# Kernel tuning notes

Measured on AMD Instinct MI355X. Metric: run time of the kernel, lower is better.

Reference implementation:

```python
import jax, jax.numpy as jnp
import numpy as np

L = 2          # num_layers
D = 2048       # embed_dim
HQ = 16        # num_q_heads
HK = 4         # num_kv_heads
HD = D // HQ   # head_size = 128
G = HQ // HK   # q_to_kv_ratio = 4
P = 8192       # embed_dim_proj
V = 32000      # vocab_size
B = 1
S = 2048
EPS = 1e-5
THETA = 500000.0
NEG = -1e30


def setup_inputs() -> dict:
    key = jax.random.key(0)
    ks = jax.random.split(key, 8)
    s = 0.02
    return {
        "tokens": jax.random.randint(ks[0], (B, S), 0, V, dtype=jnp.int32),
        "embed": jax.random.normal(ks[1], (V, D), jnp.float32) * s,
        "attn_norm_w": jnp.ones((L, D), jnp.float32),
        "qkv_w": jax.random.normal(ks[2], (L, D, D + 2 * HK * HD), jnp.float32) * s,
        "attn_out_w": jax.random.normal(ks[3], (L, D, D), jnp.float32) * s,
        "mlp_norm_w": jnp.ones((L, D), jnp.float32),
        "mlp_in_w": jax.random.normal(ks[4], (L, D, 2 * P), jnp.float32) * s,
        "mlp_out_w": jax.random.normal(ks[5], (L, P, D), jnp.float32) * s,
        "final_norm_w": jnp.ones((D,), jnp.float32),
        "lm_head_w": jax.random.normal(ks[6], (D, V), jnp.float32) * s,
    }


def _rms(x, w):
    return w * (x * jax.lax.rsqrt(jnp.mean(x * x, axis=-1, keepdims=True) + EPS))


def _rope_cos_sin():
    inv = 1.0 / (THETA ** (jnp.arange(0, HD, 2, dtype=jnp.float32) / HD))  # [HD/2]
    ang = jnp.arange(S, dtype=jnp.float32)[:, None] * inv[None, :]         # [S, HD/2]
    return jnp.cos(ang), jnp.sin(ang)


def _rope(t, cos, sin):
    # t: [B,S,H,HD]; interleaved complex rotation on (even, odd) pairs
    x = t.reshape(t.shape[:-1] + (HD // 2, 2))
    x0, x1 = x[..., 0], x[..., 1]
    c = cos[None, :, None, :]
    sn = sin[None, :, None, :]
    out = jnp.stack([x0 * c - x1 * sn, x0 * sn + x1 * c], axis=-1)
    return out.reshape(t.shape)


def _layer(x, nw1, wqkv, wo, nw2, wi, wmo, cos, sin, mask):
    # attention block (pre-norm, residual)
    h = _rms(x, nw1)
    qkv = h @ wqkv
    q = qkv[..., :D].reshape(B, S, HQ, HD)
    k = qkv[..., D:D + HK * HD].reshape(B, S, HK, HD)
    v = qkv[..., D + HK * HD:].reshape(B, S, HK, HD)
    q = _rope(q, cos, sin)
    k = _rope(k, cos, sin)
    # GQA: repeat_interleave along head dim
    k = jnp.repeat(k, G, axis=2)
    v = jnp.repeat(v, G, axis=2)
    scores = jnp.einsum('bqhd,bkhd->bhqk', q, k) / np.float32(np.sqrt(HD))
    scores = jnp.where(mask, scores, NEG)
    attn = jax.nn.softmax(scores, axis=-1)
    o = jnp.einsum('bhqk,bkhd->bqhd', attn, v).reshape(B, S, D)
    x = x + o @ wo
    # SwiGLU block (pre-norm, residual)
    h = _rms(x, nw2)
    gu = h @ wi
    gate, up = gu[..., :P], gu[..., P:]
    x = x + (jax.nn.silu(gate) * up) @ wmo
    return x


def reference(tokens, embed, attn_norm_w, qkv_w, attn_out_w, mlp_norm_w,
              mlp_in_w, mlp_out_w, final_norm_w, lm_head_w):
    cos, sin = _rope_cos_sin()
    mask = jnp.tril(jnp.ones((S, S), dtype=bool))  # offset=0 prefill -> causal
    x = embed[tokens]  # [B,S,D]
    for i in range(L):
        x = _layer(x, attn_norm_w[i], qkv_w[i], attn_out_w[i],
                   mlp_norm_w[i], mlp_in_w[i], mlp_out_w[i], cos, sin, mask)
    return _rms(x, final_norm_w) @ lm_head_w  # [B,S,V]
```

## Files before the change

### kernel.cpp

```cpp
#include <hip/hip_runtime.h>
#include <math.h>

#define S_LEN 2048
#define DMODEL 2048
#define NHQ 16
#define NHK 4
#define HDIM 128
#define PDIM 8192
#define VOCAB 32000
#define NQKV 3072
#define EPSI 1e-5f

typedef unsigned short u16;
typedef unsigned int u32;
typedef __bf16 bf16x8 __attribute__((ext_vector_type(8)));
typedef float f32x4 __attribute__((ext_vector_type(4)));

__device__ __forceinline__ u16 f2bf(float f){
  u32 u = __builtin_bit_cast(u32, f);
  u += 0x7fffu + ((u >> 16) & 1u);
  return (u16)(u >> 16);
}
__device__ __forceinline__ float bf2f(u16 h){
  u32 u = ((u32)h) << 16;
  return __builtin_bit_cast(float, u);
}
__device__ __forceinline__ bf16x8 ld8(const u16* p){
  return __builtin_bit_cast(bf16x8, *(const uint4*)p);
}
__device__ __forceinline__ f32x4 mfma16(bf16x8 a, bf16x8 b, f32x4 c){
  return __builtin_amdgcn_mfma_f32_16x16x32_bf16(a, b, c, 0, 0, 0);
}

#define GLOAD_LDS16(gp, lp) __builtin_amdgcn_global_load_lds( \
    (__attribute__((address_space(1))) void*)(gp), \
    (__attribute__((address_space(3))) void*)(lp), 16, 0, 0)

__device__ __forceinline__ bf16x8 lds_frag(const u16* Lb, int R, int g){
  const int Rp = R >> 1;
  const int s8 = (((R & 1) << 2) | g) ^ (Rp & 7);
  return ld8(Lb + Rp * 64 + s8 * 8);
}
__device__ __forceinline__ void stage_sw(const u16* base, long row0, int K, int kt,
                                         int q, u16* Ldst_waveuniform){
  const int Rp = q >> 3;
  const int u = (q & 7) ^ (Rp & 7);
  const int R = (Rp << 1) | (u >> 2);
  const u16* gp = base + (row0 + R) * (long)K + kt + ((u & 3) << 3);
  GLOAD_LDS16(gp, Ldst_waveuniform);
}

__global__ void k_embed(const int* __restrict__ tok, const float* __restrict__ emb,
                        float* __restrict__ x){
  const int s = blockIdx.x, t = threadIdx.x;
  const long r = tok[s];
  const float4* src = (const float4*)(emb + r * DMODEL);
  float4* dst = (float4*)(x + (long)s * DMODEL);
  dst[t] = src[t];
  dst[t + 256] = src[t + 256];
}

__global__ void k_rmsnorm(const float* __restrict__ x, const float* __restrict__ w,
                          u16* __restrict__ out){
  const int s = blockIdx.x, t = threadIdx.x;
  const float4* xr = (const float4*)(x + (long)s * DMODEL);
  const float4 a = xr[t], b = xr[t + 256];
  float ss = a.x*a.x + a.y*a.y + a.z*a.z + a.w*a.w
           + b.x*b.x + b.y*b.y + b.z*b.z + b.w*b.w;
  #pragma unroll
  for (int off = 32; off > 0; off >>= 1) ss += __shfl_down(ss, off, 64);
  __shared__ float part[4];
  if ((t & 63) == 0) part[t >> 6] = ss;
  __syncthreads();
  const float r = rsqrtf((part[0] + part[1] + part[2] + part[3]) * (1.f / 2048.f) + EPSI);
  const float4* wr = (const float4*)w;
  const float4 wa = wr[t], wb = wr[t + 256];
  uint2 ua, ub;
  ua.x = (u32)f2bf(a.x*r*wa.x) | ((u32)f2bf(a.y*r*wa.y) << 16);
  ua.y = (u32)f2bf(a.z*r*wa.z) | ((u32)f2bf(a.w*r*wa.w) << 16);
  ub.x = (u32)f2bf(b.x*r*wb.x) | ((u32)f2bf(b.y*r*wb.y) << 16);
  ub.y = (u32)f2bf(b.z*r*wb.z) | ((u32)f2bf(b.w*r*wb.w) << 16);
  *(uint2*)(out + (long)s * DMODEL + 4 * t) = ua;
  *(uint2*)(out + (long)s * DMODEL + 1024 + 4 * t) = ub;
}

__global__ __launch_bounds__(256) void k_convT(const float* __restrict__ W,
                                               u16* __restrict__ Wt, int N, int K){
  const int n0 = blockIdx.x * 64, k0 = blockIdx.y * 64;
  const int t = threadIdx.x;
  __shared__ u16 T[64][72];
  const int r = t >> 4, c = (t & 15) << 2;
  #pragma unroll
  for (int p = 0; p < 4; ++p){
    const int k = p * 16 + r;
    const float4 v = *(const float4*)(W + (long)(k0 + k) * N + n0 + c);
    T[c + 0][k] = f2bf(v.x);
    T[c + 1][k] = f2bf(v.y);
    T[c + 2][k] = f2bf(v.z);
    T[c + 3][k] = f2bf(v.w);
  }
  __syncthreads();
  const int nr = t >> 3, kc = (t & 7) << 3;
  #pragma unroll
  for (int p = 0; p < 2; ++p){
    const int n = p * 32 + nr;
    *(uint4*)(Wt + (long)(n0 + n) * K + k0 + kc) = *(const uint4*)(&T[n][kc]);
  }
}

__global__ __launch_bounds__(256) void k_transV(const u16* __restrict__ qkv,
                                                u16* __restrict__ vT){
  const int s0 = blockIdx.x * 64, d0 = blockIdx.y * 64, kh = blockIdx.z;
  const int t = threadIdx.x;
  __shared__ u16 T[64][72];
  #pragma unroll
  for (int p = 0; p < 4; ++p){
    const int s = p * 16 + (t >> 4);
    const int c = (t & 15) * 4;
    const uint2 v = *(const uint2*)(qkv + (long)(s0 + s) * NQKV + DMODEL + 512 + kh * HDIM + d0 + c);
    T[c + 0][s] = (u16)(v.x);
    T[c + 1][s] = (u16)(v.x >> 16);
    T[c + 2][s] = (u16)(v.y);
    T[c + 3][s] = (u16)(v.y >> 16);
  }
  __syncthreads();
  #pragma unroll
  for (int p = 0; p < 2; ++p){
    const int d = p * 32 + (t >> 3);
    *(uint4*)(vT + ((long)kh * HDIM + d0 + d) * S_LEN + s0 + (t & 7) * 8) =
        *(const uint4*)(&T[d][(t & 7) * 8]);
  }
}

template<int OUT_BF16, int RES>
__global__ __launch_bounds__(256) void k_gemm(const u16* __restrict__ A, const u16* __restrict__ Bt,
                                              void* C, const float* Rs,
                                              int M, int N, int K){
  const int bm = blockIdx.x, bn = blockIdx.y;
  const int t = threadIdx.x;
  const int w = t >> 6, lane = t & 63, l15 = lane & 15, g = lane >> 4;
  const int wr = w >> 1, wc = w & 1;
  __shared__ u16 As[4096];
  __shared__ u16 Bs[4096];
  f32x4 acc[4][4] = {};
  const long arow = (long)bm * 128;
  const long brow = (long)bn * 128;
  for (int kt = 0; kt < K; kt += 32){
    __syncthreads();
    #pragma unroll
    for (int c = 0; c < 2; ++c){
      const int q0 = ((w << 1) | c) << 6;
      const int q  = q0 | lane;
      stage_sw(A,  arow, K, kt, q, As + q0 * 8);
      stage_sw(Bt, brow, K, kt, q, Bs + q0 * 8);
    }
    __syncthreads();
    bf16x8 af[4], bfr[4];
    #pragma unroll
    for (int i = 0; i < 4; ++i)
      af[i] = lds_frag(As, wr * 64 + i * 16 + l15, g);
    #pragma unroll
    for (int i = 0; i < 4; ++i)
      bfr[i] = lds_frag(Bs, wc * 64 + i * 16 + l15, g);
    #pragma unroll
    for (int mi = 0; mi < 4; ++mi)
      #pragma unroll
      for (int ni = 0; ni < 4; ++ni)
        acc[mi][ni] = mfma16(af[mi], bfr[ni], acc[mi][ni]);
  }
  const int row0 = bm * 128 + wr * 64, col0 = bn * 128 + wc * 64;
  #pragma unroll
  for (int mi = 0; mi < 4; ++mi){
    #pragma unroll
    for (int ni = 0; ni < 4; ++ni){
      #pragma unroll
      for (int r = 0; r < 4; ++r){
        const long ri = row0 + mi * 16 + g * 4 + r;
        const long ci = col0 + ni * 16 + l15;
        float v = acc[mi][ni][r];
        if (RES) v += Rs[ri * N + ci];
        if (OUT_BF16) ((u16*)C)[ri * N + ci] = f2bf(v);
        else          ((float*)C)[ri * N + ci] = v;
      }
    }
  }
}

template<int OUT_BF16>
__global__ __launch_bounds__(512, 2) void k_gemm256(const u16* __restrict__ A,
                                                    const u16* __restrict__ Bt,
                                                    void* C, int M, int N, int K){
  __shared__ u16 L[65536];
  const int t = threadIdx.x;
  const int w = t >> 6, lane = t & 63, l15 = lane & 15, g = lane >> 4;
  const int wr = w >> 2, wc = w & 3;
  const int nbm = M >> 8;
  int id = blockIdx.x;
  {
    const int cpx = gridDim.x >> 3;
    id = (id & 7) * cpx + (id >> 3);
  }
  const int bm = id % nbm, bn = id / nbm;
  const int NT = K >> 5;

  const int Rp0 = t >> 3;
  const int u0  = (t & 7) ^ (Rp0 & 7);
  const int R0  = (Rp0 << 1) | (u0 >> 2);
  const u16* pA0 = A  + ((long)bm * 256 + R0) * (long)K + ((u0 & 3) << 3);
  const u16* pB0 = Bt + ((long)bn * 256 + R0) * (long)K + ((u0 & 3) << 3);
  const u16* pA1 = pA0 + (long)128 * K;
  const u16* pB1 = pB0 + (long)128 * K;
  const int w0 = (t & ~63) * 8;

  auto stageA = [&](int slot){
    u16* ldsA = L + slot * 8192;
    GLOAD_LDS16(pA0, ldsA + w0);
    GLOAD_LDS16(pA1, ldsA + 4096 + w0);
    pA0 += 32; pA1 += 32;
  };
  auto stageB = [&](int slot){
    u16* ldsB = L + 32768 + slot * 8192;
    GLOAD_LDS16(pB0, ldsB + w0);
    GLOAD_LDS16(pB1, ldsB + 4096 + w0);
    pB0 += 32; pB1 += 32;
  };

  #pragma unroll
  for (int i = 0; i < 3; ++i){ stageA(i); stageB(i); }
  asm volatile("s_waitcnt vmcnt(8)" ::: "memory");
  __builtin_amdgcn_s_barrier();

  f32x4 acc[8][4] = {};
  for (int tt = 0; tt < NT; ++tt){
    const u16* sA = L + (tt & 3) * 8192;
    const u16* sB = L + 32768 + (tt & 3) * 8192;
    bf16x8 af0[4], bfr[4];
    #pragma unroll
    for (int j = 0; j < 4; ++j)
      af0[j] = lds_frag(sA, wr * 128 + j * 16 + l15, g);
    #pragma unroll
    for (int n = 0; n < 4; ++n)
      bfr[n] = lds_frag(sB, wc * 64 + n * 16 + l15, g);
    if (tt + 3 < NT) stageA((tt + 3) & 3);
    asm volatile("s_waitcnt lgkmcnt(0)" ::: "memory");
    __builtin_amdgcn_s_barrier();
    __builtin_amdgcn_s_setprio(1);
    #pragma unroll
    for (int mi = 0; mi < 4; ++mi)
      #pragma unroll
      for (int ni = 0; ni < 4; ++ni)
        acc[mi][ni] = mfma16(af0[mi], bfr[ni], acc[mi][ni]);
    __builtin_amdgcn_s_setprio(0);
    bf16x8 af1[4];
    #pragma unroll
    for (int j = 0; j < 4; ++j)
      af1[j] = lds_frag(sA, wr * 128 + 64 + j * 16 + l15, g);
    if (tt + 3 < NT) stageB((tt + 3) & 3);
    asm volatile("s_waitcnt lgkmcnt(0)" ::: "memory");
    if (tt + 1 < NT){
      if (tt + 3 < NT)      asm volatile("s_waitcnt vmcnt(8)" ::: "memory");
      else if (tt + 2 < NT) asm volatile("s_waitcnt vmcnt(4)" ::: "memory");
      else                  asm volatile("s_waitcnt vmcnt(0)" ::: "memory");
    }
    __builtin_amdgcn_s_barrier();
    __builtin_amdgcn_s_setprio(1);
    #pragma unroll
    for (int mi = 0; mi < 4; ++mi)
      #pragma unroll
      for (int ni = 0; ni < 4; ++ni)
        acc[4 + mi][ni] = mfma16(af1[mi], bfr[ni], acc[4 + mi][ni]);
    __builtin_amdgcn_s_setprio(0);
  }
  const int row0 = bm * 256 + wr * 128, col0 = bn * 256 + wc * 64;
  #pragma unroll
  for (int mi = 0; mi < 8; ++mi){
    #pragma unroll
    for (int ni = 0; ni < 4; ++ni){
      #pragma unroll
      for (int r = 0; r < 4; ++r){
        const long ri = row0 + mi * 16 + g * 4 + r;
        const long ci = col0 + ni * 16 + l15;
        const float v = acc[mi][ni][r];
        if (OUT_BF16) ((u16*)C)[ri * N + ci] = f2bf(v);
        else          ((float*)C)[ri * N + ci] = v;
      }
    }
  }
}

__global__ void k_rope(u16* __restrict__ qkv){
  const int idx = blockIdx.x * 256 + threadIdx.x;
  const int i = idx & 63;
  const int head = (idx >> 6) % 20;
  const int s = idx / (64 * 20);
  const long base = (long)s * NQKV + (head < NHQ ? head * HDIM : DMODEL + (head - NHQ) * HDIM);
  u32* p = (u32*)(qkv + base + 2 * i);
  const u32 v = *p;
  const float x0 = bf2f((u16)(v & 0xffffu)), x1 = bf2f((u16)(v >> 16));
  const float ang = (float)s * exp2f(-0.29580575889569023f * (float)i);
  float sn, cs;
  sincosf(ang, &sn, &cs);
  const float y0 = x0 * cs - x1 * sn;
  const float y1 = x0 * sn + x1 * cs;
  *p = (u32)f2bf(y0) | ((u32)f2bf(y1) << 16);
}

__global__ __launch_bounds__(256) void k_attn(const u16* __restrict__ qkv,
                                              const u16* __restrict__ vT,
                                              u16* __restrict__ o){
  const int qb = blockIdx.x, h = blockIdx.y;
  const int kh = h >> 2;
  const int t = threadIdx.x, w = t >> 6, lane = t & 63, l15 = lane & 15, g = lane >> 4;
  __shared__ u16 Ks[2][8192];
  __shared__ u16 Vs[2][8192];
  __shared__ u16 Ps[4][16 * 72];
  const int q0 = qb * 64 + w * 16;
  bf16x8 aq[4];
  #pragma unroll
  for (int d0 = 0; d0 < 4; ++d0)
    aq[d0] = ld8(qkv + (long)(q0 + l15) * NQKV + h * HDIM + d0 * 32 + g * 8);
  f32x4 acc_o[8] = {};
  float mst[4], lst[4];
  #pragma unroll
  for (int r = 0; r < 4; ++r){ mst[r] = -1e30f; lst[r] = 0.f; }
  const float scale = 0.08838834764831843f;

  auto stageK = [&](int kt, int b){
    #pragma unroll
    for (int p = 0; p < 4; ++p){
      const int q = p * 256 + t;
      const int r = q >> 4, u = q & 15;
      const u16* gp = qkv + (long)(kt * 64 + r) * NQKV + DMODEL + kh * HDIM + ((u ^ (r & 15)) << 3);
      GLOAD_LDS16(gp, Ks[b] + (p * 256 + (t & ~63)) * 8);
    }
  };
  auto stageV = [&](int kt, int b){
    #pragma unroll
    for (int p = 0; p < 4; ++p){
      const int q = p * 256 + t;
      const int r = q >> 3, u = q & 7;
      const u16* gp = vT + ((long)kh * HDIM + r) * S_LEN + kt * 64 + ((u ^ (r & 7)) << 3);
      GLOAD_LDS16(gp, Vs[b] + (p * 256 + (t & ~63)) * 8);
    }
  };

  const int nkt = qb + 1;
  stageK(0, 0); stageV(0, 0);
  for (int kt = 0; kt < nkt; ++kt){
    const int kv0 = kt << 6;
    __builtin_amdgcn_s_barrier();
    if (kt + 1 < nkt){
      stageK(kt + 1, (kt + 1) & 1);
      stageV(kt + 1, (kt + 1) & 1);
      asm volatile("s_waitcnt vmcnt(8)" ::: "memory");
    } else {
      asm volatile("s_waitcnt vmcnt(0)" ::: "memory");
    }
    __builtin_amdgcn_s_barrier();
    const u16* K_ = Ks[kt & 1];
    const u16* V_ = Vs[kt & 1];
    f32x4 sacc[4] = {};
    #pragma unroll
    for (int d0 = 0; d0 < 4; ++d0){
      #pragma unroll
      for (int j = 0; j < 4; ++j){
        const bf16x8 bk = ld8(K_ + (j * 16 + l15) * 128 + ((((d0 << 2) | g) ^ l15) << 3));
        sacc[j] = mfma16(aq[d0], bk, sacc[j]);
      }
    }
    float p[4][4], scl[4];
    #pragma unroll
    for (int r = 0; r < 4; ++r){
      const int qrow = q0 + g * 4 + r;
      float mx = -1e30f;
      #pragma unroll
      for (int j = 0; j < 4; ++j){
        float sv = sacc[j][r] * scale;
        sv = (kv0 + j * 16 + l15 <= qrow) ? sv : -1e30f;
        p[j][r] = sv;
        mx = fmaxf(mx, sv);
      }
      #pragma unroll
      for (int off = 1; off < 16; off <<= 1) mx = fmaxf(mx, __shfl_xor(mx, off, 64));
      const float mnew = fmaxf(mst[r], mx);
      scl[r] = __expf(mst[r] - mnew);
      float rs = 0.f;
      #pragma unroll
      for (int j = 0; j < 4; ++j){ p[j][r] = __expf(p[j][r] - mnew); rs += p[j][r]; }
      #pragma unroll
      for (int off = 1; off < 16; off <<= 1) rs += __shfl_xor(rs, off, 64);
      lst[r] = lst[r] * scl[r] + rs;
      mst[r] = mnew;
    }
    #pragma unroll
    for (int n = 0; n < 8; ++n)
      #pragma unroll
      for (int r = 0; r < 4; ++r)
        acc_o[n][r] *= scl[r];
    #pragma unroll
    for (int j = 0; j < 4; ++j)
      #pragma unroll
      for (int r = 0; r < 4; ++r)
        Ps[w][(g * 4 + r) * 72 + j * 16 + l15] = f2bf(p[j][r]);
    #pragma unroll
    for (int kk = 0; kk < 2; ++kk){
      const bf16x8 pa = ld8(Ps[w] + l15 * 72 + kk * 32 + g * 8);
      #pragma unroll
      for (int n = 0; n < 8; ++n){
        const int row = n * 16 + l15;
        const bf16x8 bv = ld8(V_ + row * 64 + ((((kk << 2) | g) ^ (l15 & 7)) << 3));
        acc_o[n] = mfma16(pa, bv, acc_o[n]);
      }
    }
    asm volatile("s_waitcnt lgkmcnt(0)" ::: "memory");
  }
  #pragma unroll
  for (int n = 0; n < 8; ++n){
    #pragma unroll
    for (int r = 0; r < 4; ++r){
      const float ov = acc_o[n][r] / lst[r];
      o[(long)(q0 + g * 4 + r) * DMODEL + h * HDIM + n * 16 + l15] = f2bf(ov);
    }
  }
}

__global__ void k_swiglu(const u16* __restrict__ gu, u16* __restrict__ out){
  const long idx = ((long)blockIdx.x * 256 + threadIdx.x) * 8;
  const long s = idx >> 13;
  const int j = (int)(idx & 8191);
  const u16* gp = gu + s * 16384 + j;
  const uint4 gv = *(const uint4*)gp;
  const uint4 uv = *(const uint4*)(gp + PDIM);
  const u32 gw[4] = {gv.x, gv.y, gv.z, gv.w};
  const u32 uw[4] = {uv.x, uv.y, uv.z, uv.w};
  u32 ow[4];
  #pragma unroll
  for (int k = 0; k < 4; ++k){
    const float g0 = bf2f((u16)(gw[k] & 0xffffu)), g1 = bf2f((u16)(gw[k] >> 16));
    const float u0 = bf2f((u16)(uw[k] & 0xffffu)), u1 = bf2f((u16)(uw[k] >> 16));
    const float s0 = g0 / (1.f + __expf(-g0)) * u0;
    const float s1 = g1 / (1.f + __expf(-g1)) * u1;
    ow[k] = (u32)f2bf(s0) | ((u32)f2bf(s1) << 16);
  }
  uint4 ro; ro.x = ow[0]; ro.y = ow[1]; ro.z = ow[2]; ro.w = ow[3];
  *(uint4*)(out + idx) = ro;
}

extern "C" void kernel_launch(void* const* d_in, const int* in_sizes, int n_in,
                              void* d_out, int out_size, void* d_ws, size_t ws_size,
                              hipStream_t stream){
  const int*   tokens       = (const int*)d_in[0];
  const float* embed        = (const float*)d_in[1];
  const float* attn_norm_w  = (const float*)d_in[2];
  const float* qkv_w        = (const float*)d_in[3];
  const float* attn_out_w   = (const float*)d_in[4];
  const float* mlp_norm_w   = (const float*)d_in[5];
  const float* mlp_in_w     = (const float*)d_in[6];
  const float* mlp_out_w    = (const float*)d_in[7];
  const float* final_norm_w = (const float*)d_in[8];
  const float* lm_head_w    = (const float*)d_in[9];

  char* ws = (char*)d_ws;
  float* xf  = (float*)(ws);
  u16* hbf   = (u16*)(ws + 16777216);
  u16* qkvb  = (u16*)(ws + 25165824);
  u16* obf   = (u16*)(ws + 37748736);
  u16* gub   = (u16*)(ws + 46137344);
  u16* hb2   = (u16*)(ws + 113246208);
  u16* wbuf  = (u16*)(ws + 146800640);
  u16* vTb   = (u16*)(ws + 277872640);

  k_embed<<<S_LEN, 256, 0, stream>>>(tokens, embed, xf);
  for (int l = 0; l < 2; ++l){
    k_rmsnorm<<<S_LEN, 256, 0, stream>>>(xf, attn_norm_w + (long)l * DMODEL, hbf);
    k_convT<<<dim3(NQKV/64, DMODEL/64), 256, 0, stream>>>(
        qkv_w + (long)l * DMODEL * NQKV, wbuf, NQKV, DMODEL);
    k_gemm<1,0><<<dim3(S_LEN/128, NQKV/128), 256, 0, stream>>>(
        hbf, wbuf, qkvb, nullptr, S_LEN, NQKV, DMODEL);
    k_rope<<<(S_LEN * 20 * 64) / 256, 256, 0, stream>>>(qkvb);
    k_transV<<<dim3(S_LEN/64, 2, 4), 256, 0, stream>>>(qkvb, vTb);
    k_attn<<<dim3(S_LEN/64, NHQ), 256, 0, stream>>>(qkvb, vTb, obf);
    k_convT<<<dim3(DMODEL/64, DMODEL/64), 256, 0, stream>>>(
        attn_out_w + (long)l * DMODEL * DMODEL, wbuf, DMODEL, DMODEL);
    k_gemm<0,1><<<dim3(S_LEN/128, DMODEL/128), 256, 0, stream>>>(
        obf, wbuf, xf, xf, S_LEN, DMODEL, DMODEL);
    k_rmsnorm<<<S_LEN, 256, 0, stream>>>(xf, mlp_norm_w + (long)l * DMODEL, hbf);
    k_convT<<<dim3((2*PDIM)/64, DMODEL/64), 256, 0, stream>>>(
        mlp_in_w + (long)l * DMODEL * 2 * PDIM, wbuf, 2*PDIM, DMODEL);
    k_gemm256<1><<<(S_LEN/256) * ((2*PDIM)/256), 512, 0, stream>>>(
        hbf, wbuf, gub, S_LEN, 2*PDIM, DMODEL);
    k_swiglu<<<(S_LEN * PDIM / 8) / 256, 256, 0, stream>>>(gub, hb2);
    k_convT<<<dim3(DMODEL/64, PDIM/64), 256, 0, stream>>>(
        mlp_out_w + (long)l * PDIM * DMODEL, wbuf, DMODEL, PDIM);
    k_gemm<0,1><<<dim3(S_LEN/128, DMODEL/128), 256, 0, stream>>>(
        hb2, wbuf, xf, xf, S_LEN, DMODEL, PDIM);
  }
  k_rmsnorm<<<S_LEN, 256, 0, stream>>>(xf, final_norm_w, hbf);
  k_convT<<<dim3(VOCAB/64, DMODEL/64), 256, 0, stream>>>(lm_head_w, wbuf, VOCAB, DMODEL);
  k_gemm256<0><<<(S_LEN/256) * (VOCAB/256), 512, 0, stream>>>(
      hbf, wbuf, (float*)d_out, S_LEN, VOCAB, DMODEL);
}
```

Measured before the change: 1.535 ms.

## Restructure 256-tile GEMM pipeline to K=64 double-buffer and add grouped block mapping

The 256x256 GEMM mainloop moves from a 4-slot, K=32 ring buffer to a double-buffered K=64 scheme. Each iteration runs four MFMA phases separated by explicit barriers, and global-to-LDS loads for the next stage are interleaved with the fragment reads. Both GEMM kernels now use a shared XCD-aware grouped tile mapping (map_bmn) so blocks on the same XCD share A-row panels and get better L2 reuse. The small GEMM launches change from a 2D to a 1D grid with group sizes passed in. The added barriers and reduced prefetch depth could expose memory latency, and the mapping assumes the grid size is divisible by 8.

```diff
diff --git a/kernel.cpp b/kernel.cpp
--- a/kernel.cpp
+++ b/kernel.cpp
@@ -48,6 +48,16 @@
   const int R = (Rp << 1) | (u >> 2);
   const u16* gp = base + (row0 + R) * (long)K + kt + ((u & 3) << 3);
   GLOAD_LDS16(gp, Ldst_waveuniform);
+}
+
+__device__ __forceinline__ void map_bmn(int id0, int nwg, int nbn, int G,
+                                        int& bm, int& bn){
+  const int cpx = nwg >> 3;
+  const int id = (id0 & 7) * cpx + (id0 >> 3);
+  const int bmi = id % G;
+  const int r2 = id / G;
+  bn = r2 % nbn;
+  bm = (r2 / nbn) * G + bmi;
 }
 
 __global__ void k_embed(const int* __restrict__ tok, const float* __restrict__ emb,
@@ -135,8 +145,9 @@
 template<int OUT_BF16, int RES>
 __global__ __launch_bounds__(256) void k_gemm(const u16* __restrict__ A, const u16* __restrict__ Bt,
                                               void* C, const float* Rs,
-                                              int M, int N, int K){
-  const int bm = blockIdx.x, bn = blockIdx.y;
+                                              int M, int N, int K, int nbn, int G){
+  int bm, bn;
+  map_bmn(blockIdx.x, gridDim.x, nbn, G, bm, bn);
   const int t = threadIdx.x;
   const int w = t >> 6, lane = t & 63, l15 = lane & 15, g = lane >> 4;
   const int wr = w >> 1, wc = w & 1;
@@ -194,14 +205,10 @@
   const int t = threadIdx.x;
   const int w = t >> 6, lane = t & 63, l15 = lane & 15, g = lane >> 4;
   const int wr = w >> 2, wc = w & 3;
-  const int nbm = M >> 8;
-  int id = blockIdx.x;
-  {
-    const int cpx = gridDim.x >> 3;
-    id = (id & 7) * cpx + (id >> 3);
-  }
-  const int bm = id % nbm, bn = id / nbm;
-  const int NT = K >> 5;
+  const int nbn = N >> 8;
+  int bm, bn;
+  map_bmn(blockIdx.x, gridDim.x, nbn, 2, bm, bn);
+  const int NT = K >> 6;
 
   const int Rp0 = t >> 3;
   const int u0  = (t & 7) ^ (Rp0 & 7);
@@ -212,64 +219,95 @@
   const u16* pB1 = pB0 + (long)128 * K;
   const int w0 = (t & ~63) * 8;
 
-  auto stageA = [&](int slot){
-    u16* ldsA = L + slot * 8192;
-    GLOAD_LDS16(pA0, ldsA + w0);
-    GLOAD_LDS16(pA1, ldsA + 4096 + w0);
-    pA0 += 32; pA1 += 32;
-  };
-  auto stageB = [&](int slot){
-    u16* ldsB = L + 32768 + slot * 8192;
-    GLOAD_LDS16(pB0, ldsB + w0);
-    GLOAD_LDS16(pB1, ldsB + 4096 + w0);
-    pB0 += 32; pB1 += 32;
-  };
-
-  #pragma unroll
-  for (int i = 0; i < 3; ++i){ stageA(i); stageB(i); }
-  asm volatile("s_waitcnt vmcnt(8)" ::: "memory");
+  GLOAD_LDS16(pA0,      L + w0);
+  GLOAD_LDS16(pA1,      L + w0 + 4096);
+  GLOAD_LDS16(pB0,      L + 32768 + w0);
+  GLOAD_LDS16(pB1,      L + 32768 + w0 + 4096);
+  GLOAD_LDS16(pA0 + 32, L + 8192 + w0);
+  GLOAD_LDS16(pA1 + 32, L + 8192 + w0 + 4096);
+  GLOAD_LDS16(pB0 + 32, L + 32768 + 8192 + w0);
+  GLOAD_LDS16(pB1 + 32, L + 32768 + 8192 + w0 + 4096);
+  pA0 += 64; pA1 += 64; pB0 += 64; pB1 += 64;
+  asm volatile("s_waitcnt vmcnt(4)" ::: "memory");
   __builtin_amdgcn_s_barrier();
 
   f32x4 acc[8][4] = {};
   for (int tt = 0; tt < NT; ++tt){
-    const u16* sA = L + (tt & 3) * 8192;
-    const u16* sB = L + 32768 + (tt & 3) * 8192;
-    bf16x8 af0[4], bfr[4];
-    #pragma unroll
-    for (int j = 0; j < 4; ++j)
-      af0[j] = lds_frag(sA, wr * 128 + j * 16 + l15, g);
-    #pragma unroll
-    for (int n = 0; n < 4; ++n)
-      bfr[n] = lds_frag(sB, wc * 64 + n * 16 + l15, g);
-    if (tt + 3 < NT) stageA((tt + 3) & 3);
+    const int c = tt & 1, d = c ^ 1;
+    const u16* LA0 = L + c * 16384;
+    const u16* LA1 = LA0 + 8192;
+    const u16* LB0 = L + 32768 + c * 16384;
+    const u16* LB1 = LB0 + 8192;
+    u16* SA0 = L + d * 16384;
+    u16* SA1 = SA0 + 8192;
+    u16* SB0 = L + 32768 + d * 16384;
+    u16* SB1 = SB0 + 8192;
+    const bool more = (tt + 1 < NT);
+    bf16x8 afr[4], bfr[4];
+    #pragma unroll
+    for (int i = 0; i < 4; ++i) afr[i] = lds_frag(LA0, wr * 128 + i * 16 + l15, g);
+    #pragma unroll
+    for (int i = 0; i < 4; ++i) bfr[i] = lds_frag(LB0, wc * 64 + i * 16 + l15, g);
+    if (more){ GLOAD_LDS16(pA0, SA0 + w0); GLOAD_LDS16(pA1, SA0 + w0 + 4096); }
+    __builtin_amdgcn_s_barrier();
     asm volatile("s_waitcnt lgkmcnt(0)" ::: "memory");
-    __builtin_amdgcn_s_barrier();
+    __builtin_amdgcn_sched_barrier(0);
     __builtin_amdgcn_s_setprio(1);
     #pragma unroll
     for (int mi = 0; mi < 4; ++mi)
       #pragma unroll
       for (int ni = 0; ni < 4; ++ni)
-        acc[mi][ni] = mfma16(af0[mi], bfr[ni], acc[mi][ni]);
+        acc[mi][ni] = mfma16(afr[mi], bfr[ni], acc[mi][ni]);
     __builtin_amdgcn_s_setprio(0);
-    bf16x8 af1[4];
-    #pragma unroll
-    for (int j = 0; j < 4; ++j)
-      af1[j] = lds_frag(sA, wr * 128 + 64 + j * 16 + l15, g);
-    if (tt + 3 < NT) stageB((tt + 3) & 3);
+    __builtin_amdgcn_s_barrier();
+    #pragma unroll
+    for (int i = 0; i < 4; ++i) afr[i] = lds_frag(LA0, wr * 128 + 64 + i * 16 + l15, g);
+    if (more){ GLOAD_LDS16(pB0, SB0 + w0); GLOAD_LDS16(pB1, SB0 + w0 + 4096); }
+    if (more) asm volatile("s_waitcnt vmcnt(4)" ::: "memory");
+    else      asm volatile("s_waitcnt vmcnt(0)" ::: "memory");
+    __builtin_amdgcn_s_barrier();
     asm volatile("s_waitcnt lgkmcnt(0)" ::: "memory");
-    if (tt + 1 < NT){
-      if (tt + 3 < NT)      asm volatile("s_waitcnt vmcnt(8)" ::: "memory");
-      else if (tt + 2 < NT) asm volatile("s_waitcnt vmcnt(4)" ::: "memory");
-      else                  asm volatile("s_waitcnt vmcnt(0)" ::: "memory");
-    }
-    __builtin_amdgcn_s_barrier();
+    __builtin_amdgcn_sched_barrier(0);
     __builtin_amdgcn_s_setprio(1);
     #pragma unroll
     for (int mi = 0; mi < 4; ++mi)
       #pragma unroll
       for (int ni = 0; ni < 4; ++ni)
-        acc[4 + mi][ni] = mfma16(af1[mi], bfr[ni], acc[4 + mi][ni]);
+        acc[4 + mi][ni] = mfma16(afr[mi], bfr[ni], acc[4 + mi][ni]);
     __builtin_amdgcn_s_setprio(0);
+    __builtin_amdgcn_s_barrier();
+    #pragma unroll
+    for (int i = 0; i < 4; ++i) afr[i] = lds_frag(LA1, wr * 128 + i * 16 + l15, g);
+    #pragma unroll
+    for (int i = 0; i < 4; ++i) bfr[i] = lds_frag(LB1, wc * 64 + i * 16 + l15, g);
+    if (more){ GLOAD_LDS16(pA0 + 32, SA1 + w0); GLOAD_LDS16(pA1 + 32, SA1 + w0 + 4096); }
+    __builtin_amdgcn_s_barrier();
+    asm volatile("s_waitcnt lgkmcnt(0)" ::: "memory");
+    __builtin_amdgcn_sched_barrier(0);
+    __builtin_amdgcn_s_setprio(1);
+    #pragma unroll
+    for (int mi = 0; mi < 4; ++mi)
+      #pragma unroll
+      for (int ni = 0; ni < 4; ++ni)
+        acc[mi][ni] = mfma16(afr[mi], bfr[ni], acc[mi][ni]);
+    __builtin_amdgcn_s_setprio(0);
+    __builtin_amdgcn_s_barrier();
+    #pragma unroll
+    for (int i = 0; i < 4; ++i) afr[i] = lds_frag(LA1, wr * 128 + 64 + i * 16 + l15, g);
+    if (more){ GLOAD_LDS16(pB0 + 32, SB1 + w0); GLOAD_LDS16(pB1 + 32, SB1 + w0 + 4096); }
+    if (more) asm volatile("s_waitcnt vmcnt(4)" ::: "memory");
+    __builtin_amdgcn_s_barrier();
+    asm volatile("s_waitcnt lgkmcnt(0)" ::: "memory");
+    __builtin_amdgcn_sched_barrier(0);
+    __builtin_amdgcn_s_setprio(1);
+    #pragma unroll
+    for (int mi = 0; mi < 4; ++mi)
+      #pragma unroll
+      for (int ni = 0; ni < 4; ++ni)
+        acc[4 + mi][ni] = mfma16(afr[mi], bfr[ni], acc[4 + mi][ni]);
+    __builtin_amdgcn_s_setprio(0);
+    __builtin_amdgcn_s_barrier();
+    pA0 += 64; pA1 += 64; pB0 += 64; pB1 += 64;
   }
   const int row0 = bm * 256 + wr * 128, col0 = bn * 256 + wc * 64;
   #pragma unroll
@@ -475,15 +513,15 @@
     k_rmsnorm<<<S_LEN, 256, 0, stream>>>(xf, attn_norm_w + (long)l * DMODEL, hbf);
     k_convT<<<dim3(NQKV/64, DMODEL/64), 256, 0, stream>>>(
         qkv_w + (long)l * DMODEL * NQKV, wbuf, NQKV, DMODEL);
-    k_gemm<1,0><<<dim3(S_LEN/128, NQKV/128), 256, 0, stream>>>(
-        hbf, wbuf, qkvb, nullptr, S_LEN, NQKV, DMODEL);
+    k_gemm<1,0><<<(S_LEN/128) * (NQKV/128), 256, 0, stream>>>(
+        hbf, wbuf, qkvb, nullptr, S_LEN, NQKV, DMODEL, NQKV/128, 4);
     k_rope<<<(S_LEN * 20 * 64) / 256, 256, 0, stream>>>(qkvb);
     k_transV<<<dim3(S_LEN/64, 2, 4), 256, 0, stream>>>(qkvb, vTb);
     k_attn<<<dim3(S_LEN/64, NHQ), 256, 0, stream>>>(qkvb, vTb, obf);
     k_convT<<<dim3(DMODEL/64, DMODEL/64), 256, 0, stream>>>(
         attn_out_w + (long)l * DMODEL * DMODEL, wbuf, DMODEL, DMODEL);
-    k_gemm<0,1><<<dim3(S_LEN/128, DMODEL/128), 256, 0, stream>>>(
-        obf, wbuf, xf, xf, S_LEN, DMODEL, DMODEL);
+    k_gemm<0,1><<<(S_LEN/128) * (DMODEL/128), 256, 0, stream>>>(
+        obf, wbuf, xf, xf, S_LEN, DMODEL, DMODEL, DMODEL/128, 4);
     k_rmsnorm<<<S_LEN, 256, 0, stream>>>(xf, mlp_norm_w + (long)l * DMODEL, hbf);
     k_convT<<<dim3((2*PDIM)/64, DMODEL/64), 256, 0, stream>>>(
         mlp_in_w + (long)l * DMODEL * 2 * PDIM, wbuf, 2*PDIM, DMODEL);
@@ -492,8 +530,8 @@
     k_swiglu<<<(S_LEN * PDIM / 8) / 256, 256, 0, stream>>>(gub, hb2);
     k_convT<<<dim3(DMODEL/64, PDIM/64), 256, 0, stream>>>(
         mlp_out_w + (long)l * PDIM * DMODEL, wbuf, DMODEL, PDIM);
-    k_gemm<0,1><<<dim3(S_LEN/128, DMODEL/128), 256, 0, stream>>>(
-        hb2, wbuf, xf, xf, S_LEN, DMODEL, PDIM);
+    k_gemm<0,1><<<(S_LEN/128) * (DMODEL/128), 256, 0, stream>>>(
+        hb2, wbuf, xf, xf, S_LEN, DMODEL, PDIM, DMODEL/128, 2);
   }
   k_rmsnorm<<<S_LEN, 256, 0, stream>>>(xf, final_norm_w, hbf);
   k_convT<<<dim3(VOCAB/64, DMODEL/64), 256, 0, stream>>>(lm_head_w, wbuf, VOCAB, DMODEL);
```

After: 1.543 ms. No clear change (+0.5%).

## Add XCD-aware block remapping, persistent 256 GEMM, and heavy-first attention ordering

Applied to the files above, without the earlier changes.

Remaps GEMM block indices so that blocks landing on the same XCD (chiplet) share A/B tiles through grouped M-tiles, which is meant to improve L2 reuse. Turns the 256x256 GEMM into a persistent kernel: 256 workgroups each hold one M-tile fixed and loop over N-tiles with stride 32. Attention blocks are reassigned so that each XCD handles heads sharing a KV head, and query blocks are scheduled longest-first (causal) to reduce tail imbalance. In exchange, the persistent loop adds a per-tile prologue with no overlap between tiles and fixes the grid at 256, which may underfill the GPU or load-imbalance on the vocab GEMM (125 N-tiles over 32 slots).

```diff
diff --git a/kernel.cpp b/kernel.cpp
--- a/kernel.cpp
+++ b/kernel.cpp
@@ -48,6 +48,16 @@
   const int R = (Rp << 1) | (u >> 2);
   const u16* gp = base + (row0 + R) * (long)K + kt + ((u & 3) << 3);
   GLOAD_LDS16(gp, Ldst_waveuniform);
+}
+
+__device__ __forceinline__ void map_bmn(int id0, int nwg, int nbn, int G,
+                                        int& bm, int& bn){
+  const int cpx = nwg >> 3;
+  const int id = (id0 & 7) * cpx + (id0 >> 3);
+  const int bmi = id % G;
+  const int r2 = id / G;
+  bn = r2 % nbn;
+  bm = (r2 / nbn) * G + bmi;
 }
 
 __global__ void k_embed(const int* __restrict__ tok, const float* __restrict__ emb,
@@ -135,8 +145,9 @@
 template<int OUT_BF16, int RES>
 __global__ __launch_bounds__(256) void k_gemm(const u16* __restrict__ A, const u16* __restrict__ Bt,
                                               void* C, const float* Rs,
-                                              int M, int N, int K){
-  const int bm = blockIdx.x, bn = blockIdx.y;
+                                              int M, int N, int K, int nbn, int G){
+  int bm, bn;
+  map_bmn(blockIdx.x, gridDim.x, nbn, G, bm, bn);
   const int t = threadIdx.x;
   const int w = t >> 6, lane = t & 63, l15 = lane & 15, g = lane >> 4;
   const int wr = w >> 1, wc = w & 1;
@@ -187,102 +198,102 @@
 }
 
 template<int OUT_BF16>
-__global__ __launch_bounds__(512, 2) void k_gemm256(const u16* __restrict__ A,
-                                                    const u16* __restrict__ Bt,
-                                                    void* C, int M, int N, int K){
+__global__ __launch_bounds__(512, 2) void k_gemm256p(const u16* __restrict__ A,
+                                                     const u16* __restrict__ Bt,
+                                                     void* C, int M, int N, int K,
+                                                     int nbn){
   __shared__ u16 L[65536];
   const int t = threadIdx.x;
   const int w = t >> 6, lane = t & 63, l15 = lane & 15, g = lane >> 4;
   const int wr = w >> 2, wc = w & 3;
-  const int nbm = M >> 8;
-  int id = blockIdx.x;
-  {
-    const int cpx = gridDim.x >> 3;
-    id = (id & 7) * cpx + (id >> 3);
-  }
-  const int bm = id % nbm, bn = id / nbm;
+  const int bm   = blockIdx.x & 7;
+  const int slot = blockIdx.x >> 3;
   const int NT = K >> 5;
 
   const int Rp0 = t >> 3;
   const int u0  = (t & 7) ^ (Rp0 & 7);
   const int R0  = (Rp0 << 1) | (u0 >> 2);
-  const u16* pA0 = A  + ((long)bm * 256 + R0) * (long)K + ((u0 & 3) << 3);
-  const u16* pB0 = Bt + ((long)bn * 256 + R0) * (long)K + ((u0 & 3) << 3);
-  const u16* pA1 = pA0 + (long)128 * K;
-  const u16* pB1 = pB0 + (long)128 * K;
+  const int kcol0 = (u0 & 3) << 3;
+  const u16* pA0base = A + ((long)bm * 256 + R0) * (long)K + kcol0;
+  const u16* pA1base = pA0base + (long)128 * K;
   const int w0 = (t & ~63) * 8;
 
-  auto stageA = [&](int slot){
-    u16* ldsA = L + slot * 8192;
-    GLOAD_LDS16(pA0, ldsA + w0);
-    GLOAD_LDS16(pA1, ldsA + 4096 + w0);
-    pA0 += 32; pA1 += 32;
-  };
-  auto stageB = [&](int slot){
-    u16* ldsB = L + 32768 + slot * 8192;
-    GLOAD_LDS16(pB0, ldsB + w0);
-    GLOAD_LDS16(pB1, ldsB + 4096 + w0);
-    pB0 += 32; pB1 += 32;
-  };
-
-  #pragma unroll
-  for (int i = 0; i < 3; ++i){ stageA(i); stageB(i); }
-  asm volatile("s_waitcnt vmcnt(8)" ::: "memory");
-  __builtin_amdgcn_s_barrier();
-
-  f32x4 acc[8][4] = {};
-  for (int tt = 0; tt < NT; ++tt){
-    const u16* sA = L + (tt & 3) * 8192;
-    const u16* sB = L + 32768 + (tt & 3) * 8192;
-    bf16x8 af0[4], bfr[4];
-    #pragma unroll
-    for (int j = 0; j < 4; ++j)
-      af0[j] = lds_frag(sA, wr * 128 + j * 16 + l15, g);
-    #pragma unroll
-    for (int n = 0; n < 4; ++n)
-      bfr[n] = lds_frag(sB, wc * 64 + n * 16 + l15, g);
-    if (tt + 3 < NT) stageA((tt + 3) & 3);
-    asm volatile("s_waitcnt lgkmcnt(0)" ::: "memory");
+  for (int bn = slot; bn < nbn; bn += 32){
+    const u16* pA0 = pA0base;
+    const u16* pA1 = pA1base;
+    const u16* pB0 = Bt + ((long)bn * 256 + R0) * (long)K + kcol0;
+    const u16* pB1 = pB0 + (long)128 * K;
+
+    auto stageA = [&](int s){
+      u16* d = L + s * 8192;
+      GLOAD_LDS16(pA0, d + w0); GLOAD_LDS16(pA1, d + 4096 + w0);
+      pA0 += 32; pA1 += 32;
+    };
+    auto stageB = [&](int s){
+      u16* d = L + 32768 + s * 8192;
+      GLOAD_LDS16(pB0, d + w0); GLOAD_LDS16(pB1, d + 4096 + w0);
+      pB0 += 32; pB1 += 32;
+    };
+
     __builtin_amdgcn_s_barrier();
-    __builtin_amdgcn_s_setprio(1);
-    #pragma unroll
-    for (int mi = 0; mi < 4; ++mi)
-      #pragma unroll
-      for (int ni = 0; ni < 4; ++ni)
-        acc[mi][ni] = mfma16(af0[mi], bfr[ni], acc[mi][ni]);
-    __builtin_amdgcn_s_setprio(0);
-    bf16x8 af1[4];
-    #pragma unroll
-    for (int j = 0; j < 4; ++j)
-      af1[j] = lds_frag(sA, wr * 128 + 64 + j * 16 + l15, g);
-    if (tt + 3 < NT) stageB((tt + 3) & 3);
-    asm volatile("s_waitcnt lgkmcnt(0)" ::: "memory");
-    if (tt + 1 < NT){
-      if (tt + 3 < NT)      asm volatile("s_waitcnt vmcnt(8)" ::: "memory");
-      else if (tt + 2 < NT) asm volatile("s_waitcnt vmcnt(4)" ::: "memory");
-      else                  asm volatile("s_waitcnt vmcnt(0)" ::: "memory");
-    }
+    stageA(0); stageB(0); stageA(1); stageB(1); stageA(2); stageB(2);
+    asm volatile("s_waitcnt vmcnt(8)" ::: "memory");
     __builtin_amdgcn_s_barrier();
-    __builtin_amdgcn_s_setprio(1);
-    #pragma unroll
-    for (int mi = 0; mi < 4; ++mi)
-      #pragma unroll
-      for (int ni = 0; ni < 4; ++ni)
-        acc[4 + mi][ni] = mfma16(af1[mi], bfr[ni], acc[4 + mi][ni]);
-    __builtin_amdgcn_s_setprio(0);
-  }
-  const int row0 = bm * 256 + wr * 128, col0 = bn * 256 + wc * 64;
-  #pragma unroll
-  for (int mi = 0; mi < 8; ++mi){
-    #pragma unroll
-    for (int ni = 0; ni < 4; ++ni){
-      #pragma unroll
-      for (int r = 0; r < 4; ++r){
-        const long ri = row0 + mi * 16 + g * 4 + r;
-        const long ci = col0 + ni * 16 + l15;
-        const float v = acc[mi][ni][r];
-        if (OUT_BF16) ((u16*)C)[ri * N + ci] = f2bf(v);
-        else          ((float*)C)[ri * N + ci] = v;
+
+    f32x4 acc[8][4] = {};
+    for (int tt = 0; tt < NT; ++tt){
+      const u16* sA = L + (tt & 3) * 8192;
+      const u16* sB = L + 32768 + (tt & 3) * 8192;
+      bf16x8 af0[4], bfr[4];
+      #pragma unroll
+      for (int j = 0; j < 4; ++j)
+        af0[j] = lds_frag(sA, wr * 128 + j * 16 + l15, g);
+      #pragma unroll
+      for (int n = 0; n < 4; ++n)
+        bfr[n] = lds_frag(sB, wc * 64 + n * 16 + l15, g);
+      if (tt + 3 < NT) stageA((tt + 3) & 3);
+      asm volatile("s_waitcnt lgkmcnt(0)" ::: "memory");
+      __builtin_amdgcn_s_barrier();
+      __builtin_amdgcn_s_setprio(1);
+      #pragma unroll
+      for (int mi = 0; mi < 4; ++mi)
+        #pragma unroll
+        for (int ni = 0; ni < 4; ++ni)
+          acc[mi][ni] = mfma16(af0[mi], bfr[ni], acc[mi][ni]);
+      __builtin_amdgcn_s_setprio(0);
+      bf16x8 af1[4];
+      #pragma unroll
+      for (int j = 0; j < 4; ++j)
+        af1[j] = lds_frag(sA, wr * 128 + 64 + j * 16 + l15, g);
+      if (tt + 3 < NT) stageB((tt + 3) & 3);
+      asm volatile("s_waitcnt lgkmcnt(0)" ::: "memory");
+      if (tt + 1 < NT){
+        if (tt + 3 < NT)      asm volatile("s_waitcnt vmcnt(8)" ::: "memory");
+        else if (tt + 2 < NT) asm volatile("s_waitcnt vmcnt(4)" ::: "memory");
+        else                  asm volatile("s_waitcnt vmcnt(0)" ::: "memory");
+      }
+      __builtin_amdgcn_s_barrier();
+      __builtin_amdgcn_s_setprio(1);
+      #pragma unroll
+      for (int mi = 0; mi < 4; ++mi)
+        #pragma unroll
+        for (int ni = 0; ni < 4; ++ni)
+          acc[4 + mi][ni] = mfma16(af1[mi], bfr[ni], acc[4 + mi][ni]);
+      __builtin_amdgcn_s_setprio(0);
+    }
+    const int row0 = bm * 256 + wr * 128, col0 = bn * 256 + wc * 64;
+    #pragma unroll
+    for (int mi = 0; mi < 8; ++mi){
+      #pragma unroll
+      for (int ni = 0; ni < 4; ++ni){
+        #pragma unroll
+        for (int r = 0; r < 4; ++r){
+          const long ri = row0 + mi * 16 + g * 4 + r;
+          const long ci = col0 + ni * 16 + l15;
+          const float v = acc[mi][ni][r];
+          if (OUT_BF16) ((u16*)C)[ri * N + ci] = f2bf(v);
+          else          ((float*)C)[ri * N + ci] = v;
+        }
       }
     }
   }
@@ -308,8 +319,11 @@
 __global__ __launch_bounds__(256) void k_attn(const u16* __restrict__ qkv,
                                               const u16* __restrict__ vT,
                                               u16* __restrict__ o){
-  const int qb = blockIdx.x, h = blockIdx.y;
-  const int kh = h >> 2;
+  const int id = blockIdx.x;
+  const int xcd = id & 7, j = id >> 3;
+  const int kh = xcd >> 1;
+  const int h  = (kh << 2) + ((xcd & 1) << 1) + (j & 1);
+  const int qb = 31 - (j >> 1);
   const int t = threadIdx.x, w = t >> 6, lane = t & 63, l15 = lane & 15, g = lane >> 4;
   __shared__ u16 Ks[2][8192];
   __shared__ u16 Vs[2][8192];
@@ -363,9 +377,9 @@
     #pragma unroll
     for (int d0 = 0; d0 < 4; ++d0){
       #pragma unroll
-      for (int j = 0; j < 4; ++j){
-        const bf16x8 bk = ld8(K_ + (j * 16 + l15) * 128 + ((((d0 << 2) | g) ^ l15) << 3));
-        sacc[j] = mfma16(aq[d0], bk, sacc[j]);
+      for (int j2 = 0; j2 < 4; ++j2){
+        const bf16x8 bk = ld8(K_ + (j2 * 16 + l15) * 128 + ((((d0 << 2) | g) ^ l15) << 3));
+        sacc[j2] = mfma16(aq[d0], bk, sacc[j2]);
       }
     }
     float p[4][4], scl[4];
@@ -374,10 +388,10 @@
       const int qrow = q0 + g * 4 + r;
       float mx = -1e30f;
       #pragma unroll
-      for (int j = 0; j < 4; ++j){
-        float sv = sacc[j][r] * scale;
-        sv = (kv0 + j * 16 + l15 <= qrow) ? sv : -1e30f;
-        p[j][r] = sv;
+      for (int j2 = 0; j2 < 4; ++j2){
+        float sv = sacc[j2][r] * scale;
+        sv = (kv0 + j2 * 16 + l15 <= qrow) ? sv : -1e30f;
+        p[j2][r] = sv;
         mx = fmaxf(mx, sv);
       }
       #pragma unroll
@@ -386,7 +400,7 @@
       scl[r] = __expf(mst[r] - mnew);
       float rs = 0.f;
       #pragma unroll
-      for (int j = 0; j < 4; ++j){ p[j][r] = __expf(p[j][r] - mnew); rs += p[j][r]; }
+      for (int j2 = 0; j2 < 4; ++j2){ p[j2][r] = __expf(p[j2][r] - mnew); rs += p[j2][r]; }
       #pragma unroll
       for (int off = 1; off < 16; off <<= 1) rs += __shfl_xor(rs, off, 64);
       lst[r] = lst[r] * scl[r] + rs;
@@ -398,10 +412,10 @@
       for (int r = 0; r < 4; ++r)
         acc_o[n][r] *= scl[r];
     #pragma unroll
-    for (int j = 0; j < 4; ++j)
+    for (int j2 = 0; j2 < 4; ++j2)
       #pragma unroll
       for (int r = 0; r < 4; ++r)
-        Ps[w][(g * 4 + r) * 72 + j * 16 + l15] = f2bf(p[j][r]);
+        Ps[w][(g * 4 + r) * 72 + j2 * 16 + l15] = f2bf(p[j2][r]);
     #pragma unroll
     for (int kk = 0; kk < 2; ++kk){
       const bf16x8 pa = ld8(Ps[w] + l15 * 72 + kk * 32 + g * 8);
@@ -475,28 +489,28 @@
     k_rmsnorm<<<S_LEN, 256, 0, stream>>>(xf, attn_norm_w + (long)l * DMODEL, hbf);
     k_convT<<<dim3(NQKV/64, DMODEL/64), 256, 0, stream>>>(
         qkv_w + (long)l * DMODEL * NQKV, wbuf, NQKV, DMODEL);
-    k_gemm<1,0><<<dim3(S_LEN/128, NQKV/128), 256, 0, stream>>>(
-        hbf, wbuf, qkvb, nullptr, S_LEN, NQKV, DMODEL);
+    k_gemm<1,0><<<(S_LEN/128) * (NQKV/128), 256, 0, stream>>>(
+        hbf, wbuf, qkvb, nullptr, S_LEN, NQKV, DMODEL, NQKV/128, 4);
     k_rope<<<(S_LEN * 20 * 64) / 256, 256, 0, stream>>>(qkvb);
     k_transV<<<dim3(S_LEN/64, 2, 4), 256, 0, stream>>>(qkvb, vTb);
-    k_attn<<<dim3(S_LEN/64, NHQ), 256, 0, stream>>>(qkvb, vTb, obf);
+    k_attn<<<512, 256, 0, stream>>>(qkvb, vTb, obf);
     k_convT<<<dim3(DMODEL/64, DMODEL/64), 256, 0, stream>>>(
         attn_out_w + (long)l * DMODEL * DMODEL, wbuf, DMODEL, DMODEL);
-    k_gemm<0,1><<<dim3(S_LEN/128, DMODEL/128), 256, 0, stream>>>(
-        obf, wbuf, xf, xf, S_LEN, DMODEL, DMODEL);
+    k_gemm<0,1><<<(S_LEN/128) * (DMODEL/128), 256, 0, stream>>>(
+        obf, wbuf, xf, xf, S_LEN, DMODEL, DMODEL, DMODEL/128, 4);
     k_rmsnorm<<<S_LEN, 256, 0, stream>>>(xf, mlp_norm_w + (long)l * DMODEL, hbf);
     k_convT<<<dim3((2*PDIM)/64, DMODEL/64), 256, 0, stream>>>(
         mlp_in_w + (long)l * DMODEL * 2 * PDIM, wbuf, 2*PDIM, DMODEL);
-    k_gemm256<1><<<(S_LEN/256) * ((2*PDIM)/256), 512, 0, stream>>>(
-        hbf, wbuf, gub, S_LEN, 2*PDIM, DMODEL);
+    k_gemm256p<1><<<256, 512, 0, stream>>>(
+        hbf, wbuf, gub, S_LEN, 2*PDIM, DMODEL, (2*PDIM)/256);
     k_swiglu<<<(S_LEN * PDIM / 8) / 256, 256, 0, stream>>>(gub, hb2);
     k_convT<<<dim3(DMODEL/64, PDIM/64), 256, 0, stream>>>(
         mlp_out_w + (long)l * PDIM * DMODEL, wbuf, DMODEL, PDIM);
-    k_gemm<0,1><<<dim3(S_LEN/128, DMODEL/128), 256, 0, stream>>>(
-        hb2, wbuf, xf, xf, S_LEN, DMODEL, PDIM);
+    k_gemm<0,1><<<(S_LEN/128) * (DMODEL/128), 256, 0, stream>>>(
+        hb2, wbuf, xf, xf, S_LEN, DMODEL, PDIM, DMODEL/128, 2);
   }
   k_rmsnorm<<<S_LEN, 256, 0, stream>>>(xf, final_norm_w, hbf);
   k_convT<<<dim3(VOCAB/64, DMODEL/64), 256, 0, stream>>>(lm_head_w, wbuf, VOCAB, DMODEL);
-  k_gemm256<0><<<(S_LEN/256) * (VOCAB/256), 512, 0, stream>>>(
-      hbf, wbuf, (float*)d_out, S_LEN, VOCAB, DMODEL);
-}
+  k_gemm256p<0><<<256, 512, 0, stream>>>(
+      hbf, wbuf, (float*)d_out, S_LEN, VOCAB, DMODEL, VOCAB/256);
+}
```

Result: slower. 1.575 ms (+2.6%).
